# Kernel optimization log

Measured on AMD Instinct MI355X. Metric: run time of the kernel, lower is better.

Reference implementation:

```python
import jax, jax.numpy as jnp
import numpy as np

NUM_HEADS = 8
EPS_NORM = 1e-12
EPS_DEN = 1e-5


def _l2norm(x):
    # torch F.normalize(dim=-1): x / max(||x||_2, eps)
    n = jnp.sqrt(jnp.sum(x * x, axis=-1, keepdims=True))
    return x / jnp.maximum(n, EPS_NORM)


def _fast_attention(qs, ks, vs):
    # qs, ks, vs: (B', L, H, m) where L is the attended axis length
    qs = _l2norm(qs)
    ks = _l2norm(ks)
    L = qs.shape[1]
    # KV outer-product summed over the attended axis: (B', H, m, d)
    kvs = jnp.einsum('blhm,blhd->bhmd', ks, vs)
    num = jnp.einsum('bnhm,bhmd->bnhd', qs, kvs) + L * vs
    ks_sum = jnp.sum(ks, axis=1)                       # (B', H, m)
    den = jnp.einsum('bnhm,bhm->bnh', qs, ks_sum)[..., None] + L
    den = jnp.maximum(den, EPS_DEN)                    # clamp_min
    return num / den                                   # (B', L, H, m)


def setup_inputs() -> dict:
    key = jax.random.key(0)
    k1, k2, k3, k4 = jax.random.split(key, 4)
    B, T, N, D = 4, 24, 2048, 256
    x = jax.random.normal(k1, (B, T, N, D), dtype=jnp.float32)
    w_qkv = jax.random.normal(k2, (3 * D, D), dtype=jnp.float32) / np.sqrt(D)
    w_out = jax.random.normal(k3, (D, 2 * D), dtype=jnp.float32) / np.sqrt(2 * D)
    b_out = jax.random.normal(k4, (D,), dtype=jnp.float32) * 0.01
    return {"x": x, "w_qkv": w_qkv, "w_out": w_out, "b_out": b_out}


def reference(x, w_qkv, w_out, b_out):
    B, T, N, D = x.shape
    H = NUM_HEADS
    hd = D // H
    qkv = jnp.einsum('btnd,ed->btne', x, w_qkv)        # (B,T,N,3D), no bias
    q, k, v = jnp.split(qkv, 3, axis=-1)
    # heads: split last dim into (H, hd) chunks == reshape
    qh = q.reshape(B, T, N, H, hd)
    kh = k.reshape(B, T, N, H, hd)
    vh = v.reshape(B, T, N, H, hd)

    # spatial attention: attend over N, batch over (B*T)
    out_s = _fast_attention(qh.reshape(B * T, N, H, hd),
                            kh.reshape(B * T, N, H, hd),
                            vh.reshape(B * T, N, H, hd))
    out_s = out_s.reshape(B, T, N, D)

    # temporal attention: attend over T, batch over (B*N)
    qt = jnp.transpose(qh, (0, 2, 1, 3, 4)).reshape(B * N, T, H, hd)
    kt = jnp.transpose(kh, (0, 2, 1, 3, 4)).reshape(B * N, T, H, hd)
    vt = jnp.transpose(vh, (0, 2, 1, 3, 4)).reshape(B * N, T, H, hd)
    out_t = _fast_attention(qt, kt, vt).reshape(B, N, T, D)
    out_t = jnp.transpose(out_t, (0, 2, 1, 3))         # (B,T,N,D)

    out = jnp.concatenate([out_s, out_t], axis=-1)     # (B,T,N,2D)
    return jnp.einsum('btnf,df->btnd', out, w_out) + b_out
```

## Files before the change

### kernel.cpp

```cpp
#include <hip/hip_runtime.h>
#include <hip/hip_bf16.h>
#include <cstdint>
#include <cstddef>

#define B_   4
#define T_   24
#define NN_  2048
#define D_   256
#define H_   8
#define HD_  32
#define BT_  (B_*T_)
#define MTOK (B_*T_*NN_)

using bf16 = __hip_bfloat16;

typedef __attribute__((ext_vector_type(8))) short bf16x8;
typedef __attribute__((ext_vector_type(4))) float f32x4;

__device__ __forceinline__ float bf2f(bf16 v) { return __bfloat162float(v); }
__device__ __forceinline__ ushort f2bfu(float x) {
  bf16 t = __float2bfloat16(x);
  return *(ushort*)&t;
}
__device__ __forceinline__ float rsq_fast(float ss) {
  return __builtin_amdgcn_rsqf(fmaxf(ss, 1e-24f));
}
__device__ __forceinline__ float rcp_fast(float x) {
  return __builtin_amdgcn_rcpf(x);
}

__device__ __forceinline__ void async_copy16(const void* g, void* l) {
  __builtin_amdgcn_global_load_lds(
      (const __attribute__((address_space(1))) void*)g,
      (__attribute__((address_space(3))) void*)l,
      16, 0, 0);
}

__device__ __forceinline__ float red32(float v) {
  v += __shfl_xor(v, 1, 64);
  v += __shfl_xor(v, 2, 64);
  v += __shfl_xor(v, 4, 64);
  v += __shfl_xor(v, 8, 64);
  v += __shfl_xor(v, 16, 64);
  return v;
}

#define UNPK8(u, F0,F1,F2,F3,F4,F5,F6,F7)                       \
  const float F0 = __uint_as_float((u).x << 16);                \
  const float F1 = __uint_as_float((u).x & 0xffff0000u);        \
  const float F2 = __uint_as_float((u).y << 16);                \
  const float F3 = __uint_as_float((u).y & 0xffff0000u);        \
  const float F4 = __uint_as_float((u).z << 16);                \
  const float F5 = __uint_as_float((u).z & 0xffff0000u);        \
  const float F6 = __uint_as_float((u).w << 16);                \
  const float F7 = __uint_as_float((u).w & 0xffff0000u);

__global__ void k_convert(const float* __restrict__ in, bf16* __restrict__ out, int n4) {
  int i = blockIdx.x * blockDim.x + threadIdx.x;
  if (i < n4) {
    float4 v = ((const float4*)in)[i];
    bf16 t[4] = {__float2bfloat16(v.x), __float2bfloat16(v.y),
                 __float2bfloat16(v.z), __float2bfloat16(v.w)};
    ((ushort4*)out)[i] = *(ushort4*)t;
  }
}

template<int KD, bool OUTF32>
__global__ __launch_bounds__(256, 2)
void k_gemm(const bf16* __restrict__ A, const bf16* __restrict__ Bw,
            void* __restrict__ Cout, const float* __restrict__ bias, int ncols) {
  __shared__ bf16 As[128 * 64];
  __shared__ bf16 Bs[128 * 64];
  const int tid  = threadIdx.x;
  const int wave = tid >> 6, lane = tid & 63;
  const int quad = lane >> 4, l16 = lane & 15;
  const long row0 = (long)blockIdx.x * 128;
  const long col0 = (long)blockIdx.y * 128;
  const int wm = (wave & 1) * 64, wn = (wave >> 1) * 64;
  const int srow = lane >> 3;
  const int skb  = (lane & 7) * 8;

  f32x4 acc[4][4];
  const f32x4 z = {0.f, 0.f, 0.f, 0.f};
#pragma unroll
  for (int a = 0; a < 4; ++a)
#pragma unroll
    for (int b = 0; b < 4; ++b) acc[a][b] = z;

  for (int k0 = 0; k0 < KD; k0 += 64) {
#pragma unroll
    for (int i = 0; i < 4; ++i) {
      const int c = wave * 4 + i;
      const int r = c * 8 + srow;
      async_copy16(A  + (row0 + r) * KD + k0 + skb, (char*)As + c * 1024);
      async_copy16(Bw + (col0 + r) * KD + k0 + skb, (char*)Bs + c * 1024);
    }
    __syncthreads();
#pragma unroll
    for (int kk = 0; kk < 64; kk += 32) {
      bf16x8 af[4], bfr[4];
#pragma unroll
      for (int i = 0; i < 4; ++i)
        af[i] = *(const bf16x8*)(As + (wm + i * 16 + l16) * 64 + kk + quad * 8);
#pragma unroll
      for (int i = 0; i < 4; ++i)
        bfr[i] = *(const bf16x8*)(Bs + (wn + i * 16 + l16) * 64 + kk + quad * 8);
#pragma unroll
      for (int mi = 0; mi < 4; ++mi)
#pragma unroll
        for (int ni = 0; ni < 4; ++ni)
          acc[mi][ni] = __builtin_amdgcn_mfma_f32_16x16x32_bf16(af[mi], bfr[ni], acc[mi][ni], 0, 0, 0);
    }
    __syncthreads();
  }

#pragma unroll
  for (int mi = 0; mi < 4; ++mi)
#pragma unroll
    for (int ni = 0; ni < 4; ++ni) {
      const long colg = col0 + wn + ni * 16 + l16;
#pragma unroll
      for (int r = 0; r < 4; ++r) {
        const long rowg = row0 + wm + mi * 16 + quad * 4 + r;
        const float v = acc[mi][ni][r];
        if (OUTF32) {
          ((float*)Cout)[rowg * ncols + colg] = v + bias[colg];
        } else {
          ((bf16*)Cout)[rowg * ncols + colg] = __float2bfloat16(v);
        }
      }
    }
}

__global__ __launch_bounds__(256)
void k_spatial_stats(bf16* __restrict__ qkv, float* __restrict__ stats) {
  const int bt = blockIdx.x, h = blockIdx.y;
  const int tid = threadIdx.x;
  const int wave = tid >> 6, lane = tid & 63;
  __shared__ float lk[256][36];
  __shared__ float lv[256][36];
  const int mg = lane >> 3, dg = lane & 7;
  const int m0 = mg * 4, d0 = dg * 4;
  float acc[4][4] = {};
  float ssum[4] = {0.f, 0.f, 0.f, 0.f};

  for (int c = wave * 64; c < NN_; c += 256) {
    const size_t row = ((size_t)bt * NN_ + c + lane) * 768;
    bf16 kb[32], vb[32];
    const uint4* kp = (const uint4*)(qkv + row + 256 + h * 32);
    const uint4* vp = (const uint4*)(qkv + row + 512 + h * 32);
#pragma unroll
    for (int j = 0; j < 4; ++j) { ((uint4*)kb)[j] = kp[j]; ((uint4*)vb)[j] = vp[j]; }
    float kf[32]; float ss = 0.f;
#pragma unroll
    for (int j = 0; j < 32; ++j) { kf[j] = bf2f(kb[j]); ss += kf[j] * kf[j]; }
    const float sc = rsq_fast(ss);
#pragma unroll
    for (int j = 0; j < 32; ++j) kf[j] *= sc;
    ushort kh16[32];
#pragma unroll
    for (int j = 0; j < 32; ++j) kh16[j] = f2bfu(kf[j]);
    uint4* dstk = (uint4*)(qkv + row + 256 + h * 32);
#pragma unroll
    for (int j = 0; j < 4; ++j) dstk[j] = ((uint4*)kh16)[j];

    float vf[32];
#pragma unroll
    for (int j = 0; j < 32; ++j) vf[j] = bf2f(vb[j]);
    const int lrow = wave * 64 + lane;
#pragma unroll
    for (int j = 0; j < 8; ++j) {
      ((float4*)lk[lrow])[j] = ((float4*)kf)[j];
      ((float4*)lv[lrow])[j] = ((float4*)vf)[j];
    }
    __syncthreads();
#pragma unroll 2
    for (int t = 0; t < 64; ++t) {
      const int tr = wave * 64 + t;
      const float4 ka = *(const float4*)&lk[tr][m0];
      const float4 va = *(const float4*)&lv[tr][d0];
      const float km[4] = {ka.x, ka.y, ka.z, ka.w};
      const float vm[4] = {va.x, va.y, va.z, va.w};
#pragma unroll
      for (int i = 0; i < 4; ++i) {
        ssum[i] += km[i];
#pragma unroll
        for (int j = 0; j < 4; ++j) acc[i][j] += km[i] * vm[j];
      }
    }
    __syncthreads();
  }

  float* rbuf = (float*)lk;
  float* wb = rbuf + wave * 1056;
#pragma unroll
  for (int i = 0; i < 4; ++i) {
    float4 o = {acc[i][0], acc[i][1], acc[i][2], acc[i][3]};
    *(float4*)&wb[(m0 + i) * 32 + d0] = o;
  }
  if (dg == 0) {
#pragma unroll
    for (int i = 0; i < 4; ++i) wb[1024 + m0 + i] = ssum[i];
  }
  __syncthreads();
  float* base = stats + ((size_t)bt * H_ + h) * 1056;
  for (int e = tid; e < 1056; e += 256)
    base[e] = rbuf[e] + rbuf[1056 + e] + rbuf[2112 + e] + rbuf[3168 + e];
}

#define TCH 32
__global__ __launch_bounds__(256, 3)
void k_spatial_out(bf16* __restrict__ qkv, const float* __restrict__ stats,
                   bf16* __restrict__ concat) {
  const int c  = blockIdx.x;
  const int bt = blockIdx.y;
  const int tid = threadIdx.x;
  const int h = tid >> 5, d = tid & 31;
  __shared__ uint4 qrow4[TCH * 8 * 4];

  const float* sbase = stats + ((size_t)bt * H_ + h) * 1056;
  float kvcol[32];
#pragma unroll
  for (int m = 0; m < 32; ++m) kvcol[m] = sbase[m * 32 + d];
  float kss[32];
#pragma unroll
  for (int j = 0; j < 8; ++j) ((float4*)kss)[j] = ((const float4*)(sbase + 1024))[j];

  const size_t tok0 = (size_t)bt * NN_ + (size_t)c * TCH;
  const bf16* qp = qkv + tok0 * 768 + h * 32 + d;
  const bf16* vp = qp + 512;
  bf16* qwb = (bf16*)qp;
  bf16* cp  = concat + tok0 * 512 + h * 32 + d;

  for (int i = 0; i < TCH; i += 8) {
    float qf[8];
#pragma unroll
    for (int j = 0; j < 8; ++j)
      qf[j] = bf2f(qp[(i + j) * 768]);
#pragma unroll
    for (int j = 0; j < 8; ++j) {
      const float qss = red32(qf[j] * qf[j]);
      const float qn = qf[j] * rsq_fast(qss);
      const ushort qb = f2bfu(qn);
      ((ushort*)qrow4)[((i + j) * 8 + h) * 32 + d] = qb;
      ((ushort*)qwb)[(i + j) * 768] = qb;
    }
  }
  __syncthreads();

  for (int i = 0; i < TCH; i += 8) {
    float vf8[8];
#pragma unroll
    for (int j = 0; j < 8; ++j)
      vf8[j] = bf2f(vp[(i + j) * 768]);
#pragma unroll
    for (int j = 0; j < 8; ++j) {
      const uint4* r4 = qrow4 + ((i + j) * 8 + h) * 4;
      float num = 2048.f * vf8[j];
      float den = 2048.f;
#pragma unroll
      for (int cc = 0; cc < 4; ++cc) {
        const uint4 u = r4[cc];
        const int m0 = cc * 8;
        UNPK8(u, f0, f1, f2, f3, f4, f5, f6, f7)
        num = fmaf(f0, kvcol[m0+0], num); den = fmaf(f0, kss[m0+0], den);
        num = fmaf(f1, kvcol[m0+1], num); den = fmaf(f1, kss[m0+1], den);
        num = fmaf(f2, kvcol[m0+2], num); den = fmaf(f2, kss[m0+2], den);
        num = fmaf(f3, kvcol[m0+3], num); den = fmaf(f3, kss[m0+3], den);
        num = fmaf(f4, kvcol[m0+4], num); den = fmaf(f4, kss[m0+4], den);
        num = fmaf(f5, kvcol[m0+5], num); den = fmaf(f5, kss[m0+5], den);
        num = fmaf(f6, kvcol[m0+6], num); den = fmaf(f6, kss[m0+6], den);
        num = fmaf(f7, kvcol[m0+7], num); den = fmaf(f7, kss[m0+7], den);
      }
      den = fmaxf(den, 1e-5f);
      cp[(i + j) * 512] = __float2bfloat16(num * rcp_fast(den));
    }
  }
}

__global__ __launch_bounds__(256, 2)
void k_temporal_out(const bf16* __restrict__ qkv, bf16* __restrict__ concat) {
  const int n = blockIdx.x, b = blockIdx.y;
  const int tid = threadIdx.x;
  const int wave = tid >> 6, lane = tid & 63;
  const int h = tid >> 5, d = tid & 31;
  __shared__ uint4 rows4[384 * 4];

  {
    const int rl = lane >> 2, p = lane & 3;
#pragma unroll
    for (int q = 0; q < 6; ++q) {
      const int i = wave * 6 + q;
      const int R = i * 16 + rl;
      const int s = (R >= 192) ? 1 : 0;
      const int tt = (R - s * 192) >> 3;
      const int hh = R & 7;
      const size_t tok = ((size_t)b * T_ + tt) * NN_ + n;
      const size_t e = tok * 768 + (s ? 0 : 256) + hh * 32 + p * 8;
      async_copy16(qkv + e, (char*)rows4 + i * 1024);
    }
  }

  const size_t basev = ((size_t)b * T_ * NN_ + n) * 768 + 512 + h * 32 + d;
  const size_t tstep = (size_t)NN_ * 768;
  float vf[T_];
#pragma unroll
  for (int t = 0; t < T_; ++t) vf[t] = bf2f(qkv[basev + t * tstep]);

  __syncthreads();

  float kvcol[32], kss[32];
#pragma unroll
  for (int m = 0; m < 32; ++m) { kvcol[m] = 0.f; kss[m] = 0.f; }
#pragma unroll
  for (int t = 0; t < T_; ++t) {
    const uint4* r4 = rows4 + (t * 8 + h) * 4;
    const float v = vf[t];
#pragma unroll
    for (int cc = 0; cc < 4; ++cc) {
      const uint4 u = r4[cc];
      const int m0 = cc * 8;
      UNPK8(u, f0, f1, f2, f3, f4, f5, f6, f7)
      kvcol[m0+0] = fmaf(f0, v, kvcol[m0+0]); kss[m0+0] += f0;
      kvcol[m0+1] = fmaf(f1, v, kvcol[m0+1]); kss[m0+1] += f1;
      kvcol[m0+2] = fmaf(f2, v, kvcol[m0+2]); kss[m0+2] += f2;
      kvcol[m0+3] = fmaf(f3, v, kvcol[m0+3]); kss[m0+3] += f3;
      kvcol[m0+4] = fmaf(f4, v, kvcol[m0+4]); kss[m0+4] += f4;
      kvcol[m0+5] = fmaf(f5, v, kvcol[m0+5]); kss[m0+5] += f5;
      kvcol[m0+6] = fmaf(f6, v, kvcol[m0+6]); kss[m0+6] += f6;
      kvcol[m0+7] = fmaf(f7, v, kvcol[m0+7]); kss[m0+7] += f7;
    }
  }

#pragma unroll
  for (int t = 0; t < T_; ++t) {
    const uint4* r4 = rows4 + ((192 + t * 8 + h)) * 4;
    float num = 24.f * vf[t];
    float den = 24.f;
#pragma unroll
    for (int cc = 0; cc < 4; ++cc) {
      const uint4 u = r4[cc];
      const int m0 = cc * 8;
      UNPK8(u, f0, f1, f2, f3, f4, f5, f6, f7)
      num = fmaf(f0, kvcol[m0+0], num); den = fmaf(f0, kss[m0+0], den);
      num = fmaf(f1, kvcol[m0+1], num); den = fmaf(f1, kss[m0+1], den);
      num = fmaf(f2, kvcol[m0+2], num); den = fmaf(f2, kss[m0+2], den);
      num = fmaf(f3, kvcol[m0+3], num); den = fmaf(f3, kss[m0+3], den);
      num = fmaf(f4, kvcol[m0+4], num); den = fmaf(f4, kss[m0+4], den);
      num = fmaf(f5, kvcol[m0+5], num); den = fmaf(f5, kss[m0+5], den);
      num = fmaf(f6, kvcol[m0+6], num); den = fmaf(f6, kss[m0+6], den);
      num = fmaf(f7, kvcol[m0+7], num); den = fmaf(f7, kss[m0+7], den);
    }
    den = fmaxf(den, 1e-5f);
    const size_t tok = (size_t)(b * T_ + t) * NN_ + n;
    concat[tok * 512 + 256 + h * 32 + d] = __float2bfloat16(num * rcp_fast(den));
  }
}

extern "C" void kernel_launch(void* const* d_in, const int* in_sizes, int n_in,
                              void* d_out, int out_size, void* d_ws, size_t ws_size,
                              hipStream_t stream) {
  (void)in_sizes; (void)n_in; (void)out_size; (void)ws_size;
  const float* x     = (const float*)d_in[0];
  const float* w_qkv = (const float*)d_in[1];
  const float* w_out = (const float*)d_in[2];
  const float* b_out = (const float*)d_in[3];
  float* out = (float*)d_out;
  char* ws = (char*)d_ws;

  bf16* concat = (bf16*)(ws);
  bf16* xb     = (bf16*)(ws);
  bf16* qkv    = (bf16*)(ws + 201326592);
  float* stats = (float*)(ws + 503316480);
  bf16* wqkvb  = (bf16*)(ws + 506560512);
  bf16* woutb  = (bf16*)(ws + 506953728);

  k_convert<<<(MTOK * D_ / 4 + 255) / 256, 256, 0, stream>>>(x, xb, MTOK * D_ / 4);
  k_convert<<<(768 * 256 / 4 + 255) / 256, 256, 0, stream>>>(w_qkv, wqkvb, 768 * 256 / 4);
  k_convert<<<(256 * 512 / 4 + 255) / 256, 256, 0, stream>>>(w_out, woutb, 256 * 512 / 4);

  k_gemm<256, false><<<dim3(MTOK / 128, 768 / 128), 256, 0, stream>>>(xb, wqkvb, qkv, nullptr, 768);

  k_spatial_stats<<<dim3(BT_, H_), 256, 0, stream>>>(qkv, stats);

  k_spatial_out<<<dim3(NN_ / TCH, BT_), 256, 0, stream>>>(qkv, stats, concat);
  k_temporal_out<<<dim3(NN_, B_), 256, 0, stream>>>(qkv, concat);

  k_gemm<512, true><<<dim3(MTOK / 128, 256 / 128), 256, 0, stream>>>(concat, woutb, out, b_out, 256);
}
```

Baseline: 1.041 ms.

## Compute spatial attention output with MFMA using split-bf16 stats

Rewrites the spatial output kernel so each thread normalizes a whole token-head row with vectorized 16-byte loads instead of cross-lane shuffle reductions. It then computes the numerator and denominator matmuls with bf16 MFMA instructions, splitting the fp32 KV stats into hi and lo bf16 parts to keep precision. The chunk size grows to 64 tokens and the spatial kernel's launch bound goes from 3 to 4 blocks per CU; the temporal kernel's minimum-blocks hint is dropped. In exchange, the stats are re-read and converted per head, and the v loads and concat stores become scattered scalar accesses.

```diff
diff --git a/kernel.cpp b/kernel.cpp
--- a/kernel.cpp
+++ b/kernel.cpp
@@ -22,6 +22,9 @@
   bf16 t = __float2bfloat16(x);
   return *(ushort*)&t;
 }
+__device__ __forceinline__ float bfu2f(ushort u) {
+  return __uint_as_float((uint32_t)u << 16);
+}
 __device__ __forceinline__ float rsq_fast(float ss) {
   return __builtin_amdgcn_rsqf(fmaxf(ss, 1e-24f));
 }
@@ -34,15 +37,6 @@
       (const __attribute__((address_space(1))) void*)g,
       (__attribute__((address_space(3))) void*)l,
       16, 0, 0);
-}
-
-__device__ __forceinline__ float red32(float v) {
-  v += __shfl_xor(v, 1, 64);
-  v += __shfl_xor(v, 2, 64);
-  v += __shfl_xor(v, 4, 64);
-  v += __shfl_xor(v, 8, 64);
-  v += __shfl_xor(v, 16, 64);
-  return v;
 }
 
 #define UNPK8(u, F0,F1,F2,F3,F4,F5,F6,F7)                       \
@@ -208,77 +202,103 @@
     base[e] = rbuf[e] + rbuf[1056 + e] + rbuf[2112 + e] + rbuf[3168 + e];
 }
 
-#define TCH 32
-__global__ __launch_bounds__(256, 3)
+#define SP_CHUNK 64
+__global__ __launch_bounds__(256, 4)
 void k_spatial_out(bf16* __restrict__ qkv, const float* __restrict__ stats,
                    bf16* __restrict__ concat) {
   const int c  = blockIdx.x;
   const int bt = blockIdx.y;
   const int tid = threadIdx.x;
-  const int h = tid >> 5, d = tid & 31;
-  __shared__ uint4 qrow4[TCH * 8 * 4];
-
-  const float* sbase = stats + ((size_t)bt * H_ + h) * 1056;
-  float kvcol[32];
-#pragma unroll
-  for (int m = 0; m < 32; ++m) kvcol[m] = sbase[m * 32 + d];
-  float kss[32];
-#pragma unroll
-  for (int j = 0; j < 8; ++j) ((float4*)kss)[j] = ((const float4*)(sbase + 1024))[j];
-
-  const size_t tok0 = (size_t)bt * NN_ + (size_t)c * TCH;
-  const bf16* qp = qkv + tok0 * 768 + h * 32 + d;
-  const bf16* vp = qp + 512;
-  bf16* qwb = (bf16*)qp;
-  bf16* cp  = concat + tok0 * 512 + h * 32 + d;
-
-  for (int i = 0; i < TCH; i += 8) {
-    float qf[8];
-#pragma unroll
-    for (int j = 0; j < 8; ++j)
-      qf[j] = bf2f(qp[(i + j) * 768]);
-#pragma unroll
-    for (int j = 0; j < 8; ++j) {
-      const float qss = red32(qf[j] * qf[j]);
-      const float qn = qf[j] * rsq_fast(qss);
-      const ushort qb = f2bfu(qn);
-      ((ushort*)qrow4)[((i + j) * 8 + h) * 32 + d] = qb;
-      ((ushort*)qwb)[(i + j) * 768] = qb;
+  __shared__ bf16 qrows[8 * SP_CHUNK * 32];
+
+  const size_t tok0 = (size_t)bt * NN_ + (size_t)c * SP_CHUNK;
+
+  {
+    const int tok = tid & (SP_CHUNK - 1);
+    const int hp  = tid >> 6;
+#pragma unroll
+    for (int hh = 0; hh < 2; ++hh) {
+      const int h = hp * 2 + hh;
+      bf16* qp = qkv + (tok0 + tok) * 768 + h * 32;
+      ushort qu[32];
+#pragma unroll
+      for (int j = 0; j < 4; ++j) ((uint4*)qu)[j] = ((const uint4*)qp)[j];
+      float qf[32]; float ss = 0.f;
+#pragma unroll
+      for (int j = 0; j < 32; ++j) { qf[j] = bfu2f(qu[j]); ss = fmaf(qf[j], qf[j], ss); }
+      const float sc = rsq_fast(ss);
+      ushort qh[32];
+#pragma unroll
+      for (int j = 0; j < 32; ++j) qh[j] = f2bfu(qf[j] * sc);
+      bf16* lbase = qrows + (h * SP_CHUNK + tok) * 32;
+#pragma unroll
+      for (int s = 0; s < 4; ++s) {
+        ((uint4*)lbase)[s ^ (tok & 3)] = ((uint4*)qh)[s];
+        ((uint4*)qp)[s] = ((uint4*)qh)[s];
+      }
     }
   }
   __syncthreads();
 
-  for (int i = 0; i < TCH; i += 8) {
-    float vf8[8];
-#pragma unroll
-    for (int j = 0; j < 8; ++j)
-      vf8[j] = bf2f(vp[(i + j) * 768]);
-#pragma unroll
-    for (int j = 0; j < 8; ++j) {
-      const uint4* r4 = qrow4 + ((i + j) * 8 + h) * 4;
-      float num = 2048.f * vf8[j];
-      float den = 2048.f;
-#pragma unroll
-      for (int cc = 0; cc < 4; ++cc) {
-        const uint4 u = r4[cc];
-        const int m0 = cc * 8;
-        UNPK8(u, f0, f1, f2, f3, f4, f5, f6, f7)
-        num = fmaf(f0, kvcol[m0+0], num); den = fmaf(f0, kss[m0+0], den);
-        num = fmaf(f1, kvcol[m0+1], num); den = fmaf(f1, kss[m0+1], den);
-        num = fmaf(f2, kvcol[m0+2], num); den = fmaf(f2, kss[m0+2], den);
-        num = fmaf(f3, kvcol[m0+3], num); den = fmaf(f3, kss[m0+3], den);
-        num = fmaf(f4, kvcol[m0+4], num); den = fmaf(f4, kss[m0+4], den);
-        num = fmaf(f5, kvcol[m0+5], num); den = fmaf(f5, kss[m0+5], den);
-        num = fmaf(f6, kvcol[m0+6], num); den = fmaf(f6, kss[m0+6], den);
-        num = fmaf(f7, kvcol[m0+7], num); den = fmaf(f7, kss[m0+7], den);
-      }
-      den = fmaxf(den, 1e-5f);
-      cp[(i + j) * 512] = __float2bfloat16(num * rcp_fast(den));
-    }
-  }
-}
-
-__global__ __launch_bounds__(256, 2)
+  const int wave = tid >> 6, lane = tid & 63;
+  const int quad = lane >> 4, l16 = lane & 15;
+  const int tA = wave * 16 + l16;
+  const f32x4 z = {0.f, 0.f, 0.f, 0.f};
+
+  for (int h = 0; h < 8; ++h) {
+    const bf16x8 af = *(const bf16x8*)(qrows + (h * SP_CHUNK + tA) * 32 + ((quad ^ (tA & 3)) * 8));
+
+    const float* sb = stats + ((size_t)bt * H_ + h) * 1056;
+    bf16x8 bn_hi[2], bn_lo[2];
+#pragma unroll
+    for (int dh = 0; dh < 2; ++dh) {
+      ushort hi8[8], lo8[8];
+#pragma unroll
+      for (int j = 0; j < 8; ++j) {
+        const float v = sb[(quad * 8 + j) * 32 + dh * 16 + l16];
+        const ushort hu = f2bfu(v);
+        hi8[j] = hu;
+        lo8[j] = f2bfu(v - bfu2f(hu));
+      }
+      bn_hi[dh] = *(bf16x8*)hi8; bn_lo[dh] = *(bf16x8*)lo8;
+    }
+    bf16x8 bd_hi, bd_lo;
+    {
+      ushort hi8[8], lo8[8];
+#pragma unroll
+      for (int j = 0; j < 8; ++j) {
+        const float v = sb[1024 + quad * 8 + j];
+        const ushort hu = f2bfu(v);
+        hi8[j] = hu;
+        lo8[j] = f2bfu(v - bfu2f(hu));
+      }
+      bd_hi = *(bf16x8*)hi8; bd_lo = *(bf16x8*)lo8;
+    }
+
+    f32x4 aN0 = z, aN1 = z, aD = z;
+    aN0 = __builtin_amdgcn_mfma_f32_16x16x32_bf16(af, bn_hi[0], aN0, 0, 0, 0);
+    aN0 = __builtin_amdgcn_mfma_f32_16x16x32_bf16(af, bn_lo[0], aN0, 0, 0, 0);
+    aN1 = __builtin_amdgcn_mfma_f32_16x16x32_bf16(af, bn_hi[1], aN1, 0, 0, 0);
+    aN1 = __builtin_amdgcn_mfma_f32_16x16x32_bf16(af, bn_lo[1], aN1, 0, 0, 0);
+    aD  = __builtin_amdgcn_mfma_f32_16x16x32_bf16(af, bd_hi, aD, 0, 0, 0);
+    aD  = __builtin_amdgcn_mfma_f32_16x16x32_bf16(af, bd_lo, aD, 0, 0, 0);
+
+#pragma unroll
+    for (int r = 0; r < 4; ++r) {
+      const size_t tg = tok0 + wave * 16 + quad * 4 + r;
+      const float rden = rcp_fast(fmaxf(aD[r] + 2048.f, 1e-5f));
+#pragma unroll
+      for (int dh = 0; dh < 2; ++dh) {
+        const int d = dh * 16 + l16;
+        const float vv = bf2f(qkv[tg * 768 + 512 + h * 32 + d]);
+        const float num = (dh ? aN1[r] : aN0[r]) + 2048.f * vv;
+        concat[tg * 512 + h * 32 + d] = __float2bfloat16(num * rden);
+      }
+    }
+  }
+}
+
+__global__ __launch_bounds__(256)
 void k_temporal_out(const bf16* __restrict__ qkv, bf16* __restrict__ concat) {
   const int n = blockIdx.x, b = blockIdx.y;
   const int tid = threadIdx.x;
@@ -383,7 +403,7 @@
 
   k_spatial_stats<<<dim3(BT_, H_), 256, 0, stream>>>(qkv, stats);
 
-  k_spatial_out<<<dim3(NN_ / TCH, BT_), 256, 0, stream>>>(qkv, stats, concat);
+  k_spatial_out<<<dim3(NN_ / SP_CHUNK, BT_), 256, 0, stream>>>(qkv, stats, concat);
   k_temporal_out<<<dim3(NN_, B_), 256, 0, stream>>>(qkv, concat);
 
   k_gemm<512, true><<<dim3(MTOK / 128, 256 / 128), 256, 0, stream>>>(concat, woutb, out, b_out, 256);
```

Measured after the change: 1.023 ms. No clear change (-1.7%).
